# Performance work log

Hardware: AMD Instinct MI355X
Metric: run time of the kernel (lower is better)

## Reference

```python
import jax, jax.numpy as jnp
import numpy as np

DT = 1.0 / 252.0
GAMMA = 0.1

B, T, N, M = 64, 512, 64, 64


def setup_inputs() -> dict:
    key = jax.random.key(0)
    k1, k2, k3, k4, k5 = jax.random.split(key, 5)
    return {
        "action": jax.random.normal(k1, (B, T, N), dtype=jnp.float32),
        "mu": jax.random.normal(k2, (B, N, T), dtype=jnp.float32),
        "sigma": jax.random.normal(k3, (B, T, N, M), dtype=jnp.float32),
        "zeta": jax.random.normal(k4, (B, T, M), dtype=jnp.float32),
        "bt": jax.random.normal(k5, (T, 1), dtype=jnp.float32),
    }


def reference(action, mu, sigma, zeta, bt):
    # diagonal of bmm(action, mu) == batched dot over N per time step
    # relevant_wealth: (B, T)
    relevant_wealth = jnp.einsum('btn,bnt->bt', action, mu) + bt[:, 0][None, :]
    wealth = jnp.sum(relevant_wealth, axis=1) * DT  # (B,)
    # risk: (B, T, M)
    risk = jnp.einsum('btn,btnm->btm', action, sigma)
    # sum over t of squared L2 norm over M -> sum of squares over (T, M)
    sq = jnp.sum(jnp.square(risk + zeta), axis=(1, 2))  # (B,)
    risk_penalty = (GAMMA / 2.0) * DT * sq
    return wealth - risk_penalty  # (B,)
```

## Files before the change

kernel.cpp:

```cpp
#include <hip/hip_runtime.h>

constexpr int B = 64, T = 512, N = 64, M = 64;
#define DT_F (1.0f / 252.0f)
#define GAMMA_F 0.1f

__global__ __launch_bounds__(256) void wealth_partial_kernel(
        const float* __restrict__ action,
        const float* __restrict__ mu,
        const float* __restrict__ sigma,
        const float* __restrict__ zeta,
        const float* __restrict__ bt,
        float* __restrict__ partial) {
    __shared__ float lds_val[4];
    const int lane = threadIdx.x & 63;
    const int wave = threadIdx.x >> 6;
    const int b = blockIdx.x >> 7;
    const int t = ((blockIdx.x & 127) << 2) | wave;

    const int c = lane >> 4;
    const int g = lane & 15;

    const size_t bt_idx = (size_t)b * T + t;
    const float*  act = action + bt_idx * N;
    const float4* sg4 = (const float4*)(sigma + bt_idx * (size_t)(N * M));
    const float4* zt4 = (const float4*)(zeta + bt_idx * M);

    float a_reg = act[lane];

    float4 acc = make_float4(0.f, 0.f, 0.f, 0.f);
    const int nbase = c << 4;
#pragma unroll
    for (int i = 0; i < 16; ++i) {
        const int n = nbase + i;
        float  an = __shfl(a_reg, n);
        float4 s4 = sg4[n * 16 + g];
        acc.x += an * s4.x;
        acc.y += an * s4.y;
        acc.z += an * s4.z;
        acc.w += an * s4.w;
    }
#pragma unroll
    for (int off = 16; off <= 32; off <<= 1) {
        acc.x += __shfl_xor(acc.x, off);
        acc.y += __shfl_xor(acc.y, off);
        acc.z += __shfl_xor(acc.z, off);
        acc.w += __shfl_xor(acc.w, off);
    }

    float sq = 0.f;
    if (c == 0) {
        float4 z = zt4[g];
        float rx = acc.x + z.x;
        float ry = acc.y + z.y;
        float rz = acc.z + z.z;
        float rw = acc.w + z.w;
        sq = rx * rx + ry * ry + rz * rz + rw * rw;
    }

    float d = a_reg * mu[(size_t)b * N * T + (size_t)lane * T + t];

#pragma unroll
    for (int off = 1; off < 64; off <<= 1) {
        sq += __shfl_xor(sq, off);
        d  += __shfl_xor(d, off);
    }

    if (lane == 0)
        lds_val[wave] = DT_F * (d + bt[t]) - (0.5f * GAMMA_F * DT_F) * sq;
    __syncthreads();
    if (threadIdx.x == 0)
        partial[blockIdx.x] = lds_val[0] + lds_val[1] + lds_val[2] + lds_val[3];
}

__global__ void wealth_finalize_kernel(const float* __restrict__ partial,
                                       float* __restrict__ out) {
    const int b = threadIdx.x;
    const float4* p4 = (const float4*)(partial + b * (T / 4));
    float s = 0.f;
#pragma unroll
    for (int i = 0; i < T / 16; ++i) {
        float4 v = p4[i];
        s += v.x + v.y + v.z + v.w;
    }
    out[b] = s;
}

extern "C" void kernel_launch(void* const* d_in, const int* in_sizes, int n_in,
                              void* d_out, int out_size, void* d_ws, size_t ws_size,
                              hipStream_t stream) {
    const float* action = (const float*)d_in[0];
    const float* mu     = (const float*)d_in[1];
    const float* sigma  = (const float*)d_in[2];
    const float* zeta   = (const float*)d_in[3];
    const float* bt     = (const float*)d_in[4];
    float* out = (float*)d_out;
    float* partial = (float*)d_ws;

    wealth_partial_kernel<<<(B * T) / 4, 256, 0, stream>>>(
        action, mu, sigma, zeta, bt, partial);
    wealth_finalize_kernel<<<1, B, 0, stream>>>(partial, out);
}
```

Baseline: 690.5 us.

## Process four timesteps per wave with lane-per-M layout and readlane broadcasts

Each wave now handles four consecutive timesteps. Each lane owns one M column and accumulates over N, using readlane broadcasts of action instead of shuffles plus a cross-lane reduction of float4 partials. Sigma and zeta loads are nontemporal and scalar per lane (coalesced 256B rows). Mu is read as a float4 across the four timesteps, and the bt sum moves into the finalize kernel. The LDS and block barrier are dropped. Per-block work rises and grid size falls by four, trading parallelism for fewer reductions on a sigma-bandwidth-bound kernel.

```diff
diff --git a/kernel.cpp b/kernel.cpp
--- a/kernel.cpp
+++ b/kernel.cpp
@@ -4,85 +4,84 @@
 #define DT_F (1.0f / 252.0f)
 #define GAMMA_F 0.1f
 
+__device__ __forceinline__ float bcast(float v, int l) {
+    return __uint_as_float(__builtin_amdgcn_readlane(__float_as_uint(v), l));
+}
+
 __global__ __launch_bounds__(256) void wealth_partial_kernel(
         const float* __restrict__ action,
         const float* __restrict__ mu,
         const float* __restrict__ sigma,
         const float* __restrict__ zeta,
-        const float* __restrict__ bt,
         float* __restrict__ partial) {
-    __shared__ float lds_val[4];
     const int lane = threadIdx.x & 63;
     const int wave = threadIdx.x >> 6;
-    const int b = blockIdx.x >> 7;
-    const int t = ((blockIdx.x & 127) << 2) | wave;
+    const int b  = blockIdx.x >> 5;
+    const int t0 = ((blockIdx.x & 31) << 4) | (wave << 2);
 
-    const int c = lane >> 4;
-    const int g = lane & 15;
+    const size_t bt0 = (size_t)b * T + t0;
 
-    const size_t bt_idx = (size_t)b * T + t;
-    const float*  act = action + bt_idx * N;
-    const float4* sg4 = (const float4*)(sigma + bt_idx * (size_t)(N * M));
-    const float4* zt4 = (const float4*)(zeta + bt_idx * M);
+    const float4 mu4 = *(const float4*)(mu + ((size_t)b * N + lane) * T + t0);
 
-    float a_reg = act[lane];
+    float d_acc = 0.f, sq_acc = 0.f;
 
-    float4 acc = make_float4(0.f, 0.f, 0.f, 0.f);
-    const int nbase = c << 4;
 #pragma unroll
-    for (int i = 0; i < 16; ++i) {
-        const int n = nbase + i;
-        float  an = __shfl(a_reg, n);
-        float4 s4 = sg4[n * 16 + g];
-        acc.x += an * s4.x;
-        acc.y += an * s4.y;
-        acc.z += an * s4.z;
-        acc.w += an * s4.w;
+    for (int tt = 0; tt < 4; ++tt) {
+        const size_t bti = bt0 + tt;
+        const float* __restrict__ act = action + bti * N;
+        const float* __restrict__ sg  = sigma  + bti * (size_t)(N * M);
+
+        const float a_lane = act[lane];
+        const float mu_c = (tt == 0) ? mu4.x : (tt == 1) ? mu4.y
+                         : (tt == 2) ? mu4.z : mu4.w;
+        d_acc = fmaf(a_lane, mu_c, d_acc);
+
+        float ac0 = 0.f, ac1 = 0.f, ac2 = 0.f, ac3 = 0.f;
+#pragma unroll
+        for (int n = 0; n < N; n += 4) {
+            ac0 = fmaf(bcast(a_lane, n + 0),
+                       __builtin_nontemporal_load(sg + (n + 0) * M + lane), ac0);
+            ac1 = fmaf(bcast(a_lane, n + 1),
+                       __builtin_nontemporal_load(sg + (n + 1) * M + lane), ac1);
+            ac2 = fmaf(bcast(a_lane, n + 2),
+                       __builtin_nontemporal_load(sg + (n + 2) * M + lane), ac2);
+            ac3 = fmaf(bcast(a_lane, n + 3),
+                       __builtin_nontemporal_load(sg + (n + 3) * M + lane), ac3);
+        }
+        const float r = ((ac0 + ac1) + (ac2 + ac3))
+                      + __builtin_nontemporal_load(zeta + bti * M + lane);
+        sq_acc = fmaf(r, r, sq_acc);
     }
-#pragma unroll
-    for (int off = 16; off <= 32; off <<= 1) {
-        acc.x += __shfl_xor(acc.x, off);
-        acc.y += __shfl_xor(acc.y, off);
-        acc.z += __shfl_xor(acc.z, off);
-        acc.w += __shfl_xor(acc.w, off);
-    }
-
-    float sq = 0.f;
-    if (c == 0) {
-        float4 z = zt4[g];
-        float rx = acc.x + z.x;
-        float ry = acc.y + z.y;
-        float rz = acc.z + z.z;
-        float rw = acc.w + z.w;
-        sq = rx * rx + ry * ry + rz * rz + rw * rw;
-    }
-
-    float d = a_reg * mu[(size_t)b * N * T + (size_t)lane * T + t];
 
 #pragma unroll
     for (int off = 1; off < 64; off <<= 1) {
-        sq += __shfl_xor(sq, off);
-        d  += __shfl_xor(d, off);
+        d_acc  += __shfl_xor(d_acc,  off);
+        sq_acc += __shfl_xor(sq_acc, off);
     }
-
     if (lane == 0)
-        lds_val[wave] = DT_F * (d + bt[t]) - (0.5f * GAMMA_F * DT_F) * sq;
-    __syncthreads();
-    if (threadIdx.x == 0)
-        partial[blockIdx.x] = lds_val[0] + lds_val[1] + lds_val[2] + lds_val[3];
+        partial[(blockIdx.x << 2) | wave] =
+            DT_F * d_acc - (0.5f * GAMMA_F * DT_F) * sq_acc;
 }
 
 __global__ void wealth_finalize_kernel(const float* __restrict__ partial,
+                                       const float* __restrict__ bt,
                                        float* __restrict__ out) {
     const int b = threadIdx.x;
+    float bts = 0.f;
+    const float4* bt4 = (const float4*)bt;
+#pragma unroll
+    for (int i = 0; i < T / 4; ++i) {
+        float4 v = bt4[i];
+        bts += (v.x + v.y) + (v.z + v.w);
+    }
     const float4* p4 = (const float4*)(partial + b * (T / 4));
     float s = 0.f;
 #pragma unroll
     for (int i = 0; i < T / 16; ++i) {
         float4 v = p4[i];
-        s += v.x + v.y + v.z + v.w;
+        s += (v.x + v.y) + (v.z + v.w);
     }
-    out[b] = s;
+    out[b] = s + DT_F * bts;
 }
 
 extern "C" void kernel_launch(void* const* d_in, const int* in_sizes, int n_in,
@@ -96,7 +95,7 @@
     float* out = (float*)d_out;
     float* partial = (float*)d_ws;
 
-    wealth_partial_kernel<<<(B * T) / 4, 256, 0, stream>>>(
-        action, mu, sigma, zeta, bt, partial);
-    wealth_finalize_kernel<<<1, B, 0, stream>>>(partial, out);
+    wealth_partial_kernel<<<(B * T) / 16, 256, 0, stream>>>(
+        action, mu, sigma, zeta, partial);
+    wealth_finalize_kernel<<<1, B, 0, stream>>>(partial, bt, out);
 }
```

Measured after the change: 690.4 us. About the same (-0.0%).
